# Kernel tuning notes

Hardware: AMD Instinct MI355X
Metric: run time of the kernel (lower is better)

Reference implementation:

```python
import jax, jax.numpy as jnp
import numpy as np
jax.config.update('jax_enable_x64', True)

B, S, D, H, V, P = 4, 2048, 512, 8, 100000, 256
NGRAMS = list(range(3, 9))  # n-gram lengths 3..8
DH = D // H
SCALE = np.float32(DH ** -0.5)

def _layernorm(x, g, b, eps=1e-5):
    m = jnp.mean(x, -1, keepdims=True)
    v = jnp.mean(jnp.square(x - m), -1, keepdims=True)
    return g * (x - m) / jnp.sqrt(v + eps) + b

def _mha(q, k, v, Wq, bq, Wk, bk, Wv, bv, Wo, bo):
    Bq, Lq, _ = q.shape
    qh = (q @ Wq + bq).reshape(Bq, Lq, H, DH)
    kh = (k @ Wk + bk).reshape(Bq, -1, H, DH)
    vh = (v @ Wv + bv).reshape(Bq, -1, H, DH)
    s = jnp.einsum('bqhd,bkhd->bhqk', qh, kh) * SCALE
    a = jax.nn.softmax(s, axis=-1)
    o = jnp.einsum('bhqk,bkhd->bqhd', a, vh).reshape(Bq, Lq, D)
    return o @ Wo + bo

def _ngram_hash(bytes_seq, n):
    # hash[:, i] = sum_k bytes[:, i-n+1+k] * 256**k for i >= n-1 else 0, then mod V
    # (int64 wraparound for n=8 matches torch semantics)
    b = bytes_seq.astype(jnp.int64)
    h = jnp.zeros_like(b)
    for k in range(n):
        shift = n - 1 - k
        shifted = jnp.pad(b, ((0, 0), (shift, 0)))[:, :S]
        h = h + shifted * (256 ** k)
    h = jnp.where(jnp.arange(S) >= (n - 1), h, 0)
    return h % V

def _forward(bytes_seq, patch_idx, byte_emb, ngram_emb, sWq, sbq, sWk, sbk, sWv, sbv, sWo, sbo, ln1g, ln1b, W1, b1, W2, b2, ln2g, ln2b, cWq, cbq, cWk, cbk, cWv, cbv, cWo, cbo):
    embeds = byte_emb[bytes_seq]  # [B,S,D]
    for j, n in enumerate(NGRAMS):
        embeds = embeds + ngram_emb[j][_ngram_hash(bytes_seq, n)]
    embeds = embeds / np.float32(len(NGRAMS) + 1)
    # one post-norm transformer encoder layer (relu FFN, eval mode / no dropout)
    x = _layernorm(embeds + _mha(embeds, embeds, embeds, sWq, sbq, sWk, sbk, sWv, sbv, sWo, sbo), ln1g, ln1b)
    ff = jax.nn.relu(x @ W1 + b1) @ W2 + b2
    x = _layernorm(x + ff, ln2g, ln2b)
    # gather patch-boundary queries per batch, cross-attend to full sequence
    q = jnp.take_along_axis(x, patch_idx[..., None], axis=1)  # [B,P,D]
    return _mha(q, x, x, cWq, cbq, cWk, cbk, cWv, cbv, cWo, cbo)

def setup_inputs():
    key = jax.random.key(0)
    ks = jax.random.split(key, 20)
    f32 = jnp.float32
    def rn(k, shape, scale=0.02):
        return (jax.random.normal(k, shape, f32) * scale).astype(f32)
    return {
        'bytes_seq': jax.random.randint(ks[0], (B, S), 0, 256, dtype=jnp.int64),
        'patch_idx': jnp.sort(jax.random.randint(ks[1], (B, P), 0, S, dtype=jnp.int64), axis=1),
        'byte_emb': rn(ks[2], (256, D)),
        'ngram_emb': rn(ks[3], (len(NGRAMS), V, D)),
        'sWq': rn(ks[4], (D, D)), 'sbq': jnp.zeros((D,), f32),
        'sWk': rn(ks[5], (D, D)), 'sbk': jnp.zeros((D,), f32),
        'sWv': rn(ks[6], (D, D)), 'sbv': jnp.zeros((D,), f32),
        'sWo': rn(ks[7], (D, D)), 'sbo': jnp.zeros((D,), f32),
        'ln1g': jnp.ones((D,), f32), 'ln1b': jnp.zeros((D,), f32),
        'W1': rn(ks[8], (D, 4 * D)), 'b1': jnp.zeros((4 * D,), f32),
        'W2': rn(ks[9], (4 * D, D)), 'b2': jnp.zeros((D,), f32),
        'ln2g': jnp.ones((D,), f32), 'ln2b': jnp.zeros((D,), f32),
        'cWq': rn(ks[10], (D, D)), 'cbq': jnp.zeros((D,), f32),
        'cWk': rn(ks[11], (D, D)), 'cbk': jnp.zeros((D,), f32),
        'cWv': rn(ks[12], (D, D)), 'cbv': jnp.zeros((D,), f32),
        'cWo': rn(ks[13], (D, D)), 'cbo': jnp.zeros((D,), f32),
    }

def reference(bytes_seq, patch_idx, byte_emb, ngram_emb, sWq, sbq, sWk, sbk, sWv, sbv, sWo, sbo, ln1g, ln1b, W1, b1, W2, b2, ln2g, ln2b, cWq, cbq, cWk, cbk, cWv, cbv, cWo, cbo):
    return _forward(bytes_seq, patch_idx, byte_emb, ngram_emb, sWq, sbq, sWk, sbk, sWv, sbv, sWo, sbo, ln1g, ln1b, W1, b1, W2, b2, ln2g, ln2b, cWq, cbq, cWk, cbk, cWv, cbv, cWo, cbo)
```

## Files before the change

kernel.cpp:

```cpp
#include <hip/hip_runtime.h>
#include <stdint.h>

#define B_   4
#define S_   2048
#define D_   512
#define H_   8
#define DH_  64
#define V_   100000
#define P_   256
#define N_   (B_*S_)
#define NP_  (B_*P_)

typedef _Float16 f16;
typedef _Float16 f16x8 __attribute__((ext_vector_type(8)));
typedef float    f32x4 __attribute__((ext_vector_type(4)));
typedef uint32_t u32x4 __attribute__((ext_vector_type(4)));

#define MFMA16(a,b,c) __builtin_amdgcn_mfma_f32_16x16x32_f16((a),(b),(c),0,0,0)
#define GLDS16(gp, lp) __builtin_amdgcn_global_load_lds( \
    (const __attribute__((address_space(1))) void*)(gp), \
    (__attribute__((address_space(3))) void*)(lp), 16, 0, 0)

__global__ __launch_bounds__(128) void embed_kernel(
    const int* __restrict__ bytes_seq, const float* __restrict__ byte_emb,
    const float* __restrict__ ngram_emb, f16* __restrict__ out16)
{
  const int pos = blockIdx.x;
  const int b = pos / S_, s = pos % S_;
  const int* bs = bytes_seq + (size_t)b * S_;

  int w[8];
  #pragma unroll
  for (int k = 0; k < 8; k++) {
    int p = s - 7 + k;
    w[k] = (p >= 0) ? bs[p] : 0;
  }

  int idx[6];
  #pragma unroll
  for (int j = 0; j < 6; j++) {
    const int n = j + 3;
    int id = 0;
    if (s >= n - 1) {
      uint64_t h = 0;
      for (int k = 0; k < n; k++)
        h += (uint64_t)(uint32_t)w[8 - n + k] << (8 * k);
      long long sh = (long long)h;
      long long r = sh % (long long)V_;
      if (r < 0) r += V_;
      id = (int)r;
    }
    idx[j] = id;
  }

  const int d = threadIdx.x * 4;
  float4 acc = *(const float4*)(byte_emb + (size_t)bs[s] * D_ + d);
  #pragma unroll
  for (int j = 0; j < 6; j++) {
    const float4 v = *(const float4*)(ngram_emb + ((size_t)j * V_ + idx[j]) * D_ + d);
    acc.x += v.x; acc.y += v.y; acc.z += v.z; acc.w += v.w;
  }
  const float inv7 = 1.0f / 7.0f;
  f16* o16 = out16 + (size_t)pos * D_ + d;
  f16 t4[4];
  t4[0] = (f16)(acc.x * inv7); t4[1] = (f16)(acc.y * inv7);
  t4[2] = (f16)(acc.z * inv7); t4[3] = (f16)(acc.w * inv7);
  *(uint2*)o16 = *(uint2*)t4;
}

struct WJobs {
  const float* src[10];
  f16* dst[10];
  int K[10], N[10], tiles[10];
};

__global__ __launch_bounds__(256) void wconv_kernel(WJobs jobs,
    const float* sbq, const float* sbk, const float* sbv,
    const float* cbk, const float* cbv, float* bqkv, float* bckv)
{
  const int j = blockIdx.y;
  const int tile = blockIdx.x;
  if (j == 0 && tile >= jobs.tiles[0] && tile < jobs.tiles[0] + 10) {
    int t = (tile - jobs.tiles[0]) * 256 + threadIdx.x;
    if (t < 512)       bqkv[t] = sbq[t];
    else if (t < 1024) bqkv[t] = sbk[t - 512];
    else if (t < 1536) bqkv[t] = sbv[t - 1024];
    else if (t < 2048) bckv[t - 1536] = cbk[t - 1536];
    else if (t < 2560) bckv[t - 1536] = cbv[t - 2048];
    return;
  }
  if (tile >= jobs.tiles[j]) return;
  const int K = jobs.K[j], N = jobs.N[j];
  const int ntiles = N >> 5;
  const int kt = (tile / ntiles) << 5, nt = (tile % ntiles) << 5;
  __shared__ float T[32][33];
  const int t = threadIdx.x;
  const float* src = jobs.src[j];
  #pragma unroll
  for (int p = 0; p < 4; p++) {
    int lin = t + p * 256;
    int rr = lin >> 5, cc = lin & 31;
    T[rr][cc] = src[(size_t)(kt + rr) * N + nt + cc];
  }
  __syncthreads();
  f16* dst = jobs.dst[j];
  #pragma unroll
  for (int p = 0; p < 4; p++) {
    int lin = t + p * 256;
    int rr = lin >> 5, cc = lin & 31;
    dst[(size_t)(nt + rr) * K + kt + cc] = (f16)T[cc][rr];
  }
}

template<typename OutT, int RELU, int BN>
__global__ __launch_bounds__(256) void gemm_f16(
    const f16* __restrict__ A, const f16* __restrict__ Bt,
    const float* __restrict__ bias, OutT* __restrict__ C,
    int M, int N, int K, const int* __restrict__ rowmap)
{
  constexpr int NF = BN / 32;
  __shared__ __align__(16) f16 As[2][128 * 32];
  __shared__ __align__(16) f16 Bs[2][BN * 32];
  const int tid = threadIdx.x;
  const int l = tid & 63;
  const int lo4 = l & 15, hi2 = l >> 4;
  const int w = tid >> 6;
  const int wr = w >> 1, wc = w & 1;
  const int bm = blockIdx.x * 128, bn = blockIdx.y * BN;

  size_t aoff[2];
  #pragma unroll
  for (int i = 0; i < 2; i++) {
    int r = bm + i * 64 + (tid >> 2);
    int ar = rowmap ? ((r >> 8) * S_ + rowmap[r]) : r;
    aoff[i] = (size_t)ar * K + (tid & 3) * 8;
  }

  f32x4 acc[4][NF];
  #pragma unroll
  for (int m = 0; m < 4; m++)
    #pragma unroll
    for (int n = 0; n < NF; n++) acc[m][n] = (f32x4){0.f, 0.f, 0.f, 0.f};

  const int nt = K >> 5;

  #pragma unroll
  for (int i = 0; i < 2; i++)
    GLDS16(A + aoff[i], &As[0][(i * 256 + tid) * 8]);
  #pragma unroll
  for (int i = 0; i < BN / 64; i++) {
    int c = i * 256 + tid;
    GLDS16(Bt + (size_t)(bn + (c >> 2)) * K + (c & 3) * 8, &Bs[0][c * 8]);
  }

  for (int t = 0; t < nt; t++) {
    __syncthreads();
    const int cur = t & 1;
    if (t + 1 < nt) {
      const int k0 = (t + 1) << 5;
      #pragma unroll
      for (int i = 0; i < 2; i++)
        GLDS16(A + aoff[i] + k0, &As[cur ^ 1][(i * 256 + tid) * 8]);
      #pragma unroll
      for (int i = 0; i < BN / 64; i++) {
        int c = i * 256 + tid;
        GLDS16(Bt + (size_t)(bn + (c >> 2)) * K + k0 + (c & 3) * 8, &Bs[cur ^ 1][c * 8]);
      }
    }
    f16x8 af[4], bf[NF];
    const f16* pa = &As[cur][(wr * 64 + lo4) * 32 + hi2 * 8];
    const f16* pb = &Bs[cur][(wc * (BN / 2) + lo4) * 32 + hi2 * 8];
    #pragma unroll
    for (int m = 0; m < 4; m++) af[m] = *(const f16x8*)(pa + m * 16 * 32);
    #pragma unroll
    for (int n = 0; n < NF; n++) bf[n] = *(const f16x8*)(pb + n * 16 * 32);
    #pragma unroll
    for (int m = 0; m < 4; m++)
      #pragma unroll
      for (int n = 0; n < NF; n++)
        acc[m][n] = MFMA16(af[m], bf[n], acc[m][n]);
  }

  #pragma unroll
  for (int n = 0; n < NF; n++) {
    const int col = bn + wc * (BN / 2) + n * 16 + lo4;
    const float bcol = bias[col];
    #pragma unroll
    for (int m = 0; m < 4; m++) {
      const int row0 = bm + wr * 64 + m * 16 + hi2 * 4;
      #pragma unroll
      for (int j = 0; j < 4; j++) {
        float v = acc[m][n][j] + bcol;
        if (RELU) v = fmaxf(v, 0.f);
        C[(size_t)(row0 + j) * N + col] = (OutT)v;
      }
    }
  }
}

template<int QG>
__global__ __launch_bounds__(256) void attn_f16(
    const f16* __restrict__ Q, int qs,
    const f16* __restrict__ Kp, const f16* __restrict__ Vp, int kvs,
    f16* __restrict__ O, int NQ)
{
  __shared__ __align__(16) f16 Ks[2][64][76];
  __shared__ __align__(16) f16 Vt[2][64][76];

  const int tid = threadIdx.x;
  const int w = tid >> 6, l = tid & 63;
  const int lo4 = l & 15, hi2 = l >> 4;
  const int lin = blockIdx.x;
  const int h = lin & 7, b = (lin >> 3) & 3, qt = lin >> 5;

  const f16 qscale = (f16)0.18033688f;
  f16x8 qf[QG][2];
  #pragma unroll
  for (int qg = 0; qg < QG; qg++) {
    const int qrow = qt * (64 * QG) + w * (16 * QG) + qg * 16 + lo4;
    const f16* Qp = Q + (size_t)(b * NQ + qrow) * qs + h * DH_ + hi2 * 8;
    qf[qg][0] = *(const f16x8*)(Qp);
    qf[qg][1] = *(const f16x8*)(Qp + 32);
    #pragma unroll
    for (int i = 0; i < 8; i++) { qf[qg][0][i] *= qscale; qf[qg][1][i] *= qscale; }
  }

  const int g2 = lo4 >> 2, j4 = lo4 & 3;
  const int kvp0 = 8 * g2 + j4;
  const int kvp1 = 8 * (g2 ^ 2) + 4 + j4;
  const int pidx = (l ^ 32) << 2;

  const f16* Kb = Kp + (size_t)b * S_ * kvs + h * DH_;
  const f16* Vb = Vp + (size_t)b * S_ * kvs + h * DH_;

  float lsum[QG];
  f32x4 oacc[QG][4];
  #pragma unroll
  for (int qg = 0; qg < QG; qg++) {
    lsum[qg] = 0.f;
    #pragma unroll
    for (int df = 0; df < 4; df++) oacc[qg][df] = (f32x4){0.f, 0.f, 0.f, 0.f};
  }

  const int r0 = tid >> 3;
  const int c8 = tid & 7;

  f16x8 kreg[2], vreg[2];
  #pragma unroll
  for (int i = 0; i < 2; i++) {
    int row = i * 32 + r0;
    kreg[i] = *(const f16x8*)(Kb + (size_t)row * kvs + c8 * 8);
    vreg[i] = *(const f16x8*)(Vb + (size_t)row * kvs + c8 * 8);
  }
  #pragma unroll
  for (int i = 0; i < 2; i++) {
    int row = i * 32 + r0;
    *(f16x8*)(&Ks[0][row][c8 * 8]) = kreg[i];
    #pragma unroll
    for (int jj = 0; jj < 8; jj++) Vt[0][c8 * 8 + jj][row] = vreg[i][jj];
  }
  __syncthreads();

  const int NT = S_ / 64;
  int cur = 0;
  for (int t = 0; t < NT; t++) {
    if (t + 1 < NT) {
      #pragma unroll
      for (int i = 0; i < 2; i++) {
        int row = (t + 1) * 64 + i * 32 + r0;
        kreg[i] = *(const f16x8*)(Kb + (size_t)row * kvs + c8 * 8);
        vreg[i] = *(const f16x8*)(Vb + (size_t)row * kvs + c8 * 8);
      }
    }
    f32x4 sacc[QG][4];
    #pragma unroll
    for (int nf = 0; nf < 4; nf++) {
      const int krow = ((nf & 1) ? kvp1 : kvp0) + (nf >> 1) * 32;
      f16x8 kf0 = *(const f16x8*)(&Ks[cur][krow][hi2 * 8]);
      f16x8 kf1 = *(const f16x8*)(&Ks[cur][krow][32 + hi2 * 8]);
      #pragma unroll
      for (int qg = 0; qg < QG; qg++) {
        f32x4 s = (f32x4){0.f, 0.f, 0.f, 0.f};
        s = MFMA16(kf0, qf[qg][0], s);
        s = MFMA16(kf1, qf[qg][1], s);
        sacc[qg][nf] = s;
      }
    }
    uint32_t packs[QG][4][2];
    #pragma unroll
    for (int qg = 0; qg < QG; qg++)
      #pragma unroll
      for (int nf = 0; nf < 4; nf++) {
        float p0 = exp2f(fminf(sacc[qg][nf][0], 15.f));
        float p1 = exp2f(fminf(sacc[qg][nf][1], 15.f));
        float p2 = exp2f(fminf(sacc[qg][nf][2], 15.f));
        float p3 = exp2f(fminf(sacc[qg][nf][3], 15.f));
        lsum[qg] += (p0 + p1) + (p2 + p3);
        packs[qg][nf][0] = __builtin_bit_cast(uint32_t, __builtin_amdgcn_cvt_pkrtz(p0, p1));
        packs[qg][nf][1] = __builtin_bit_cast(uint32_t, __builtin_amdgcn_cvt_pkrtz(p2, p3));
      }
    #pragma unroll
    for (int ks = 0; ks < 2; ks++) {
      f16x8 pb[QG];
      #pragma unroll
      for (int qg = 0; qg < QG; qg++) {
        uint32_t w0 = packs[qg][2 * ks][0];
        uint32_t w1 = packs[qg][2 * ks][1];
        uint32_t w2 = (uint32_t)__builtin_amdgcn_ds_bpermute(pidx, (int)packs[qg][2 * ks + 1][0]);
        uint32_t w3 = (uint32_t)__builtin_amdgcn_ds_bpermute(pidx, (int)packs[qg][2 * ks + 1][1]);
        u32x4 bw = (u32x4){w0, w1, w2, w3};
        pb[qg] = __builtin_bit_cast(f16x8, bw);
      }
      #pragma unroll
      for (int df = 0; df < 4; df++) {
        f16x8 vf = *(const f16x8*)(&Vt[cur][df * 16 + lo4][ks * 32 + hi2 * 8]);
        #pragma unroll
        for (int qg = 0; qg < QG; qg++)
          oacc[qg][df] = MFMA16(vf, pb[qg], oacc[qg][df]);
      }
    }
    if (t + 1 < NT) {
      #pragma unroll
      for (int i = 0; i < 2; i++) {
        int row = i * 32 + r0;
        *(f16x8*)(&Ks[cur ^ 1][row][c8 * 8]) = kreg[i];
        #pragma unroll
        for (int jj = 0; jj < 8; jj++) Vt[cur ^ 1][c8 * 8 + jj][row] = vreg[i][jj];
      }
    }
    __syncthreads();
    cur ^= 1;
  }

  #pragma unroll
  for (int qg = 0; qg < QG; qg++) {
    float r = lsum[qg];
    r += __shfl_xor(r, 16, 64);
    r += __shfl_xor(r, 32, 64);
    const float invl = 1.0f / r;
    const int orow = qt * (64 * QG) + w * (16 * QG) + qg * 16 + lo4;
    f16* Ob = O + (size_t)(b * NQ + orow) * D_ + h * DH_ + hi2 * 4;
    #pragma unroll
    for (int df = 0; df < 4; df++) {
      f16 t4[4];
      #pragma unroll
      for (int j = 0; j < 4; j++) t4[j] = (f16)(oacc[qg][df][j] * invl);
      *(uint2*)(Ob + df * 16) = *(uint2*)t4;
    }
  }
}

__global__ __launch_bounds__(128) void ln_kernel(
    const f16* __restrict__ a, const f16* __restrict__ r,
    const float* __restrict__ g, const float* __restrict__ be,
    f16* __restrict__ out)
{
  const int row = blockIdx.x;
  const int t = threadIdx.x;
  const f16* ap = a + (size_t)row * D_ + t * 4;
  const f16* rp = r + (size_t)row * D_ + t * 4;
  uint2 au = *(const uint2*)ap, ru = *(const uint2*)rp;
  f16 a4[4], r4[4];
  *(uint2*)a4 = au; *(uint2*)r4 = ru;
  float x0 = (float)a4[0] + (float)r4[0];
  float x1 = (float)a4[1] + (float)r4[1];
  float x2 = (float)a4[2] + (float)r4[2];
  float x3 = (float)a4[3] + (float)r4[3];
  float sm = x0 + x1 + x2 + x3;
  float sq = x0*x0 + x1*x1 + x2*x2 + x3*x3;
  #pragma unroll
  for (int off = 32; off > 0; off >>= 1) {
    sm += __shfl_down(sm, off, 64);
    sq += __shfl_down(sq, off, 64);
  }
  __shared__ float s0[2], s1[2];
  if ((t & 63) == 0) { s0[t >> 6] = sm; s1[t >> 6] = sq; }
  __syncthreads();
  const float Sm = s0[0] + s0[1];
  const float Sq = s1[0] + s1[1];
  const float mean = Sm * (1.0f / 512.0f);
  const float var  = Sq * (1.0f / 512.0f) - mean * mean;
  const float inv  = rsqrtf(var + 1e-5f);
  const float4 vg = *(const float4*)(g + t * 4);
  const float4 vb = *(const float4*)(be + t * 4);
  f16 o4[4];
  o4[0] = (f16)(vg.x * (x0 - mean) * inv + vb.x);
  o4[1] = (f16)(vg.y * (x1 - mean) * inv + vb.y);
  o4[2] = (f16)(vg.z * (x2 - mean) * inv + vb.z);
  o4[3] = (f16)(vg.w * (x3 - mean) * inv + vb.w);
  *(uint2*)(out + (size_t)row * D_ + t * 4) = *(uint2*)o4;
}

extern "C" void kernel_launch(void* const* d_in, const int* in_sizes, int n_in,
                              void* d_out, int out_size, void* d_ws, size_t ws_size,
                              hipStream_t stream) {
  const int*   bytes_seq = (const int*)  d_in[0];
  const int*   patch_idx = (const int*)  d_in[1];
  const float* byte_emb  = (const float*)d_in[2];
  const float* ngram_emb = (const float*)d_in[3];
  const float* sWq = (const float*)d_in[4];  const float* sbq = (const float*)d_in[5];
  const float* sWk = (const float*)d_in[6];  const float* sbk = (const float*)d_in[7];
  const float* sWv = (const float*)d_in[8];  const float* sbv = (const float*)d_in[9];
  const float* sWo = (const float*)d_in[10]; const float* sbo = (const float*)d_in[11];
  const float* ln1g = (const float*)d_in[12]; const float* ln1b = (const float*)d_in[13];
  const float* W1 = (const float*)d_in[14];  const float* b1 = (const float*)d_in[15];
  const float* W2 = (const float*)d_in[16];  const float* b2 = (const float*)d_in[17];
  const float* ln2g = (const float*)d_in[18]; const float* ln2b = (const float*)d_in[19];
  const float* cWq = (const float*)d_in[20]; const float* cbq = (const float*)d_in[21];
  const float* cWk = (const float*)d_in[22]; const float* cbk = (const float*)d_in[23];
  const float* cWv = (const float*)d_in[24]; const float* cbv = (const float*)d_in[25];
  const float* cWo = (const float*)d_in[26]; const float* cbo = (const float*)d_in[27];

  char* base = (char*)d_ws;
  const size_t MB = 1u << 20;
  f16* E16     = (f16*)(base + 0 * MB);
  f16* TMP16   = (f16*)(base + 8 * MB);
  f16* X116    = (f16*)(base + 16 * MB);
  f16* X216    = (f16*)(base + 24 * MB);
  f16* QKV16   = (f16*)(base + 32 * MB);
  f16* AT16    = (f16*)(base + 56 * MB);
  f16* HID16   = (f16*)(base + 64 * MB);
  f16* CKV16   = (f16*)(base + 96 * MB);
  f16* CQ16    = (f16*)(base + 112 * MB);
  f16* CO16    = (f16*)(base + 113 * MB);
  f16* WT      = (f16*)(base + 114 * MB);
  float* bqkv  = (float*)(base + 123 * MB);
  float* bckv  = bqkv + 1536;

  f16* QKVT = WT;
  f16* sWoT = QKVT + 786432;
  f16* W1T  = sWoT + 262144;
  f16* W2T  = W1T + 1048576;
  f16* cWqT = W2T + 1048576;
  f16* CKVT = cWqT + 262144;
  f16* cWoT = CKVT + 524288;

  WJobs wj;
  {
    const float* wsrc[10] = {sWq, sWk, sWv, sWo, W1, W2, cWq, cWk, cWv, cWo};
    f16* wdst[10] = {QKVT, QKVT + 262144, QKVT + 524288, sWoT, W1T, W2T,
                     cWqT, CKVT, CKVT + 262144, cWoT};
    const int wK[10] = {512,512,512,512, 512,2048, 512,512,512,512};
    const int wN[10] = {512,512,512,512, 2048,512, 512,512,512,512};
    for (int i = 0; i < 10; i++) {
      wj.src[i] = wsrc[i]; wj.dst[i] = wdst[i];
      wj.K[i] = wK[i]; wj.N[i] = wN[i];
      wj.tiles[i] = (wK[i] >> 5) * (wN[i] >> 5);
    }
  }

  const dim3 blk256(256), blk128(128);

  wconv_kernel<<<dim3(1024, 10), blk256, 0, stream>>>(wj, sbq, sbk, sbv, cbk, cbv, bqkv, bckv);
  embed_kernel<<<N_, blk128, 0, stream>>>(bytes_seq, byte_emb, ngram_emb, E16);

  gemm_f16<f16, 0, 128><<<dim3(64, 12), blk256, 0, stream>>>(E16, QKVT, bqkv, QKV16, N_, 1536, 512, nullptr);

  attn_f16<2><<<512, blk256, 0, stream>>>(QKV16, 1536, QKV16 + 512, QKV16 + 1024, 1536, AT16, S_);

  gemm_f16<f16, 0, 64><<<dim3(64, 8), blk256, 0, stream>>>(AT16, sWoT, sbo, TMP16, N_, 512, 512, nullptr);
  ln_kernel<<<N_, blk128, 0, stream>>>(E16, TMP16, ln1g, ln1b, X116);

  gemm_f16<f16, 1, 128><<<dim3(64, 16), blk256, 0, stream>>>(X116, W1T, b1, HID16, N_, 2048, 512, nullptr);
  gemm_f16<f16, 0, 64><<<dim3(64, 8), blk256, 0, stream>>>(HID16, W2T, b2, TMP16, N_, 512, 2048, nullptr);
  ln_kernel<<<N_, blk128, 0, stream>>>(X116, TMP16, ln2g, ln2b, X216);

  gemm_f16<f16, 0, 128><<<dim3(64, 8), blk256, 0, stream>>>(X216, CKVT, bckv, CKV16, N_, 1024, 512, nullptr);
  gemm_f16<f16, 0, 64><<<dim3(8, 8), blk256, 0, stream>>>(X216, cWqT, cbq, CQ16, NP_, 512, 512, patch_idx);
  attn_f16<1><<<128, blk256, 0, stream>>>(CQ16, 512, CKV16, CKV16 + 512, 1024, CO16, P_);

  gemm_f16<float, 0, 64><<<dim3(8, 8), blk256, 0, stream>>>(CO16, cWoT, cbo, (float*)d_out, NP_, 512, 512, nullptr);
}
```

Baseline: 287.4 us.

## Emit transposed V from GEMM epilogue, merge prep and cross-attn projection kernels

The QKV and cross-KV GEMM epilogues now write V in a per-(batch,head) transposed layout, so the attention kernel loads V tiles straight into LDS with global_load_lds and an XOR swizzle. This replaces the register round trip and scalar transposed LDS stores it used before. Weight conversion, bias copy and embedding are merged into one prep kernel, and the cross K/V and Q projections share one launch. The cost is extra workspace and scattered 8-byte stores in the GEMM epilogue.

```diff
diff --git a/kernel.cpp b/kernel.cpp
--- a/kernel.cpp
+++ b/kernel.cpp
@@ -21,11 +21,58 @@
     (const __attribute__((address_space(1))) void*)(gp), \
     (__attribute__((address_space(3))) void*)(lp), 16, 0, 0)
 
-__global__ __launch_bounds__(128) void embed_kernel(
+struct WJobs {
+  const float* src[10];
+  f16* dst[10];
+  int K[10], N[10], tiles[10];
+};
+
+__global__ __launch_bounds__(256) void prep_kernel(WJobs jobs,
+    const float* __restrict__ sbq, const float* __restrict__ sbk,
+    const float* __restrict__ sbv, const float* __restrict__ cbk,
+    const float* __restrict__ cbv, float* __restrict__ bqkv,
+    float* __restrict__ bckv,
     const int* __restrict__ bytes_seq, const float* __restrict__ byte_emb,
     const float* __restrict__ ngram_emb, f16* __restrict__ out16)
 {
-  const int pos = blockIdx.x;
+  int bid = blockIdx.x;
+  if (bid < 10240) {
+    const int j = bid >> 10, tile = bid & 1023;
+    if (tile >= jobs.tiles[j]) return;
+    const int K = jobs.K[j], N = jobs.N[j];
+    const int ntiles = N >> 5;
+    const int kt = (tile / ntiles) << 5, nt = (tile % ntiles) << 5;
+    __shared__ float T[32][33];
+    const int t = threadIdx.x;
+    const float* src = jobs.src[j];
+    #pragma unroll
+    for (int p = 0; p < 4; p++) {
+      int lin = t + p * 256;
+      int rr = lin >> 5, cc = lin & 31;
+      T[rr][cc] = src[(size_t)(kt + rr) * N + nt + cc];
+    }
+    __syncthreads();
+    f16* dst = jobs.dst[j];
+    #pragma unroll
+    for (int p = 0; p < 4; p++) {
+      int lin = t + p * 256;
+      int rr = lin >> 5, cc = lin & 31;
+      dst[(size_t)(nt + rr) * K + kt + cc] = (f16)T[cc][rr];
+    }
+    return;
+  }
+  bid -= 10240;
+  if (bid < 10) {
+    int t = bid * 256 + threadIdx.x;
+    if (t < 512)       bqkv[t] = sbq[t];
+    else if (t < 1024) bqkv[t] = sbk[t - 512];
+    else if (t < 1536) bqkv[t] = sbv[t - 1024];
+    else if (t < 2048) bckv[t - 1536] = cbk[t - 1536];
+    else if (t < 2560) bckv[t - 1536] = cbv[t - 2048];
+    return;
+  }
+  bid -= 10;
+  const int pos = bid * 2 + (threadIdx.x >> 7);
   const int b = pos / S_, s = pos % S_;
   const int* bs = bytes_seq + (size_t)b * S_;
 
@@ -35,7 +82,6 @@
     int p = s - 7 + k;
     w[k] = (p >= 0) ? bs[p] : 0;
   }
-
   int idx[6];
   #pragma unroll
   for (int j = 0; j < 6; j++) {
@@ -52,8 +98,7 @@
     }
     idx[j] = id;
   }
-
-  const int d = threadIdx.x * 4;
+  const int d = (threadIdx.x & 127) * 4;
   float4 acc = *(const float4*)(byte_emb + (size_t)bs[s] * D_ + d);
   #pragma unroll
   for (int j = 0; j < 6; j++) {
@@ -61,62 +106,18 @@
     acc.x += v.x; acc.y += v.y; acc.z += v.z; acc.w += v.w;
   }
   const float inv7 = 1.0f / 7.0f;
-  f16* o16 = out16 + (size_t)pos * D_ + d;
   f16 t4[4];
   t4[0] = (f16)(acc.x * inv7); t4[1] = (f16)(acc.y * inv7);
   t4[2] = (f16)(acc.z * inv7); t4[3] = (f16)(acc.w * inv7);
-  *(uint2*)o16 = *(uint2*)t4;
-}
-
-struct WJobs {
-  const float* src[10];
-  f16* dst[10];
-  int K[10], N[10], tiles[10];
-};
-
-__global__ __launch_bounds__(256) void wconv_kernel(WJobs jobs,
-    const float* sbq, const float* sbk, const float* sbv,
-    const float* cbk, const float* cbv, float* bqkv, float* bckv)
-{
-  const int j = blockIdx.y;
-  const int tile = blockIdx.x;
-  if (j == 0 && tile >= jobs.tiles[0] && tile < jobs.tiles[0] + 10) {
-    int t = (tile - jobs.tiles[0]) * 256 + threadIdx.x;
-    if (t < 512)       bqkv[t] = sbq[t];
-    else if (t < 1024) bqkv[t] = sbk[t - 512];
-    else if (t < 1536) bqkv[t] = sbv[t - 1024];
-    else if (t < 2048) bckv[t - 1536] = cbk[t - 1536];
-    else if (t < 2560) bckv[t - 1536] = cbv[t - 2048];
-    return;
-  }
-  if (tile >= jobs.tiles[j]) return;
-  const int K = jobs.K[j], N = jobs.N[j];
-  const int ntiles = N >> 5;
-  const int kt = (tile / ntiles) << 5, nt = (tile % ntiles) << 5;
-  __shared__ float T[32][33];
-  const int t = threadIdx.x;
-  const float* src = jobs.src[j];
-  #pragma unroll
-  for (int p = 0; p < 4; p++) {
-    int lin = t + p * 256;
-    int rr = lin >> 5, cc = lin & 31;
-    T[rr][cc] = src[(size_t)(kt + rr) * N + nt + cc];
-  }
-  __syncthreads();
-  f16* dst = jobs.dst[j];
-  #pragma unroll
-  for (int p = 0; p < 4; p++) {
-    int lin = t + p * 256;
-    int rr = lin >> 5, cc = lin & 31;
-    dst[(size_t)(nt + rr) * K + kt + cc] = (f16)T[cc][rr];
-  }
-}
-
-template<typename OutT, int RELU, int BN>
-__global__ __launch_bounds__(256) void gemm_f16(
+  *(uint2*)(out16 + (size_t)pos * D_ + d) = *(uint2*)t4;
+}
+
+template<typename OutT, int RELU, int BN, int VTSTART>
+__device__ __forceinline__ void gemm_body(
     const f16* __restrict__ A, const f16* __restrict__ Bt,
     const float* __restrict__ bias, OutT* __restrict__ C,
-    int M, int N, int K, const int* __restrict__ rowmap)
+    int M, int N, int K, const int* __restrict__ rowmap,
+    f16* __restrict__ vt, int bmi, int bni)
 {
   constexpr int NF = BN / 32;
   __shared__ __align__(16) f16 As[2][128 * 32];
@@ -126,7 +127,7 @@
   const int lo4 = l & 15, hi2 = l >> 4;
   const int w = tid >> 6;
   const int wr = w >> 1, wc = w & 1;
-  const int bm = blockIdx.x * 128, bn = blockIdx.y * BN;
+  const int bm = bmi * 128, bn = bni * BN;
 
   size_t aoff[2];
   #pragma unroll
@@ -181,6 +182,27 @@
         acc[m][n] = MFMA16(af[m], bf[n], acc[m][n]);
   }
 
+  if constexpr (VTSTART >= 0) {
+    if (bn >= VTSTART) {
+      #pragma unroll
+      for (int n = 0; n < NF; n++) {
+        const int col = bn + wc * (BN / 2) + n * 16 + lo4;
+        const float bcol = bias[col];
+        const int dcol = col - VTSTART;
+        const size_t vbase = ((size_t)(dcol >> 6) * 64 + (dcol & 63)) << 11;
+        #pragma unroll
+        for (int m = 0; m < 4; m++) {
+          const int row0 = bm + wr * 64 + m * 16 + hi2 * 4;
+          f16 t4[4];
+          #pragma unroll
+          for (int j = 0; j < 4; j++) t4[j] = (f16)(acc[m][n][j] + bcol);
+          *(uint2*)(vt + (((size_t)(row0 >> 11) * 8) << 17) + vbase + (row0 & 2047)) = *(uint2*)t4;
+        }
+      }
+      return;
+    }
+  }
+
   #pragma unroll
   for (int n = 0; n < NF; n++) {
     const int col = bn + wc * (BN / 2) + n * 16 + lo4;
@@ -198,14 +220,42 @@
   }
 }
 
+template<typename OutT, int RELU, int BN, int VTSTART>
+__global__ __launch_bounds__(256) void gemm_f16(
+    const f16* __restrict__ A, const f16* __restrict__ Bt,
+    const float* __restrict__ bias, OutT* __restrict__ C,
+    int M, int N, int K, const int* __restrict__ rowmap, f16* __restrict__ vt)
+{
+  gemm_body<OutT, RELU, BN, VTSTART>(A, Bt, bias, C, M, N, K, rowmap, vt,
+                                     blockIdx.x, blockIdx.y);
+}
+
+__global__ __launch_bounds__(256) void ckv_cq_kernel(
+    const f16* __restrict__ X, const f16* __restrict__ CKVT,
+    const float* __restrict__ bckv, f16* __restrict__ CKV,
+    f16* __restrict__ vt2, const f16* __restrict__ cWqT,
+    const float* __restrict__ cbq, f16* __restrict__ CQ,
+    const int* __restrict__ pidx)
+{
+  int bid = blockIdx.x;
+  if (bid < 512) {
+    gemm_body<f16, 0, 128, 512>(X, CKVT, bckv, CKV, N_, 1024, 512,
+                                nullptr, vt2, bid >> 3, bid & 7);
+  } else {
+    bid -= 512;
+    gemm_body<f16, 0, 64, -1>(X, cWqT, cbq, CQ, NP_, 512, 512,
+                              pidx, nullptr, bid >> 3, bid & 7);
+  }
+}
+
 template<int QG>
 __global__ __launch_bounds__(256) void attn_f16(
     const f16* __restrict__ Q, int qs,
-    const f16* __restrict__ Kp, const f16* __restrict__ Vp, int kvs,
-    f16* __restrict__ O, int NQ)
+    const f16* __restrict__ Kp, int kvs,
+    const f16* __restrict__ VT, f16* __restrict__ O, int NQ)
 {
   __shared__ __align__(16) f16 Ks[2][64][76];
-  __shared__ __align__(16) f16 Vt[2][64][76];
+  __shared__ __align__(16) f16 VtL[2][64 * 64];
 
   const int tid = threadIdx.x;
   const int w = tid >> 6, l = tid & 63;
@@ -229,9 +279,10 @@
   const int kvp0 = 8 * g2 + j4;
   const int kvp1 = 8 * (g2 ^ 2) + 4 + j4;
   const int pidx = (l ^ 32) << 2;
+  const int vswz = lo4 & 7;
 
   const f16* Kb = Kp + (size_t)b * S_ * kvs + h * DH_;
-  const f16* Vb = Vp + (size_t)b * S_ * kvs + h * DH_;
+  const f16* VTbh = VT + (((size_t)(b * 8 + h)) << 17);
 
   float lsum[QG];
   f32x4 oacc[QG][4];
@@ -244,33 +295,37 @@
 
   const int r0 = tid >> 3;
   const int c8 = tid & 7;
-
-  f16x8 kreg[2], vreg[2];
+  const int vr = tid >> 3;
+  const int vch = tid & 7;
+
   #pragma unroll
   for (int i = 0; i < 2; i++) {
-    int row = i * 32 + r0;
-    kreg[i] = *(const f16x8*)(Kb + (size_t)row * kvs + c8 * 8);
-    vreg[i] = *(const f16x8*)(Vb + (size_t)row * kvs + c8 * 8);
-  }
-  #pragma unroll
-  for (int i = 0; i < 2; i++) {
-    int row = i * 32 + r0;
-    *(f16x8*)(&Ks[0][row][c8 * 8]) = kreg[i];
-    #pragma unroll
-    for (int jj = 0; jj < 8; jj++) Vt[0][c8 * 8 + jj][row] = vreg[i][jj];
-  }
+    int r = i * 32 + vr, ch = vch;
+    GLDS16(VTbh + (size_t)r * 2048 + ((ch ^ (r & 7)) * 8), &VtL[0][(i * 256 + tid) * 8]);
+  }
+  f16x8 kreg[2];
+  #pragma unroll
+  for (int i = 0; i < 2; i++)
+    kreg[i] = *(const f16x8*)(Kb + (size_t)(i * 32 + r0) * kvs + c8 * 8);
+  #pragma unroll
+  for (int i = 0; i < 2; i++)
+    *(f16x8*)(&Ks[0][i * 32 + r0][c8 * 8]) = kreg[i];
   __syncthreads();
 
   const int NT = S_ / 64;
   int cur = 0;
   for (int t = 0; t < NT; t++) {
     if (t + 1 < NT) {
+      const int kt2 = (t + 1) * 64;
       #pragma unroll
       for (int i = 0; i < 2; i++) {
-        int row = (t + 1) * 64 + i * 32 + r0;
-        kreg[i] = *(const f16x8*)(Kb + (size_t)row * kvs + c8 * 8);
-        vreg[i] = *(const f16x8*)(Vb + (size_t)row * kvs + c8 * 8);
-      }
+        int r = i * 32 + vr;
+        GLDS16(VTbh + (size_t)r * 2048 + kt2 + ((vch ^ (r & 7)) * 8),
+               &VtL[cur ^ 1][(i * 256 + tid) * 8]);
+      }
+      #pragma unroll
+      for (int i = 0; i < 2; i++)
+        kreg[i] = *(const f16x8*)(Kb + (size_t)(kt2 + i * 32 + r0) * kvs + c8 * 8);
     }
     f32x4 sacc[QG][4];
     #pragma unroll
@@ -313,7 +368,9 @@
       }
       #pragma unroll
       for (int df = 0; df < 4; df++) {
-        f16x8 vf = *(const f16x8*)(&Vt[cur][df * 16 + lo4][ks * 32 + hi2 * 8]);
+        const int r = df * 16 + lo4;
+        const int cc = (ks * 4 + hi2) ^ vswz;
+        f16x8 vf = *(const f16x8*)(&VtL[cur][r * 64 + cc * 8]);
         #pragma unroll
         for (int qg = 0; qg < QG; qg++)
           oacc[qg][df] = MFMA16(vf, pb[qg], oacc[qg][df]);
@@ -321,12 +378,8 @@
     }
     if (t + 1 < NT) {
       #pragma unroll
-      for (int i = 0; i < 2; i++) {
-        int row = i * 32 + r0;
-        *(f16x8*)(&Ks[cur ^ 1][row][c8 * 8]) = kreg[i];
-        #pragma unroll
-        for (int jj = 0; jj < 8; jj++) Vt[cur ^ 1][c8 * 8 + jj][row] = vreg[i][jj];
-      }
+      for (int i = 0; i < 2; i++)
+        *(f16x8*)(&Ks[cur ^ 1][i * 32 + r0][c8 * 8]) = kreg[i];
     }
     __syncthreads();
     cur ^= 1;
@@ -426,6 +479,8 @@
   f16* WT      = (f16*)(base + 114 * MB);
   float* bqkv  = (float*)(base + 123 * MB);
   float* bckv  = bqkv + 1536;
+  f16* VT      = (f16*)(base + 124 * MB);
+  f16* VT2     = (f16*)(base + 132 * MB);
 
   f16* QKVT = WT;
   f16* sWoT = QKVT + 786432;
@@ -451,23 +506,29 @@
 
   const dim3 blk256(256), blk128(128);
 
-  wconv_kernel<<<dim3(1024, 10), blk256, 0, stream>>>(wj, sbq, sbk, sbv, cbk, cbv, bqkv, bckv);
-  embed_kernel<<<N_, blk128, 0, stream>>>(bytes_seq, byte_emb, ngram_emb, E16);
-
-  gemm_f16<f16, 0, 128><<<dim3(64, 12), blk256, 0, stream>>>(E16, QKVT, bqkv, QKV16, N_, 1536, 512, nullptr);
-
-  attn_f16<2><<<512, blk256, 0, stream>>>(QKV16, 1536, QKV16 + 512, QKV16 + 1024, 1536, AT16, S_);
-
-  gemm_f16<f16, 0, 64><<<dim3(64, 8), blk256, 0, stream>>>(AT16, sWoT, sbo, TMP16, N_, 512, 512, nullptr);
+  prep_kernel<<<10240 + 10 + 4096, blk256, 0, stream>>>(
+      wj, sbq, sbk, sbv, cbk, cbv, bqkv, bckv,
+      bytes_seq, byte_emb, ngram_emb, E16);
+
+  gemm_f16<f16, 0, 128, 1024><<<dim3(64, 12), blk256, 0, stream>>>(
+      E16, QKVT, bqkv, QKV16, N_, 1536, 512, nullptr, VT);
+
+  attn_f16<2><<<512, blk256, 0, stream>>>(QKV16, 1536, QKV16 + 512, 1536, VT, AT16, S_);
+
+  gemm_f16<f16, 0, 64, -1><<<dim3(64, 8), blk256, 0, stream>>>(
+      AT16, sWoT, sbo, TMP16, N_, 512, 512, nullptr, nullptr);
   ln_kernel<<<N_, blk128, 0, stream>>>(E16, TMP16, ln1g, ln1b, X116);
 
-  gemm_f16<f16, 1, 128><<<dim3(64, 16), blk256, 0, stream>>>(X116, W1T, b1, HID16, N_, 2048, 512, nullptr);
-  gemm_f16<f16, 0, 64><<<dim3(64, 8), blk256, 0, stream>>>(HID16, W2T, b2, TMP16, N_, 512, 2048, nullptr);
+  gemm_f16<f16, 1, 128, -1><<<dim3(64, 16), blk256, 0, stream>>>(
+      X116, W1T, b1, HID16, N_, 2048, 512, nullptr, nullptr);
+  gemm_f16<f16, 0, 64, -1><<<dim3(64, 8), blk256, 0, stream>>>(
+      HID16, W2T, b2, TMP16, N_, 512, 2048, nullptr, nullptr);
   ln_kernel<<<N_, blk128, 0, stream>>>(X116, TMP16, ln2g, ln2b, X216);
 
-  gemm_f16<f16, 0, 128><<<dim3(64, 8), blk256, 0, stream>>>(X216, CKVT, bckv, CKV16, N_, 1024, 512, nullptr);
-  gemm_f16<f16, 0, 64><<<dim3(8, 8), blk256, 0, stream>>>(X216, cWqT, cbq, CQ16, NP_, 512, 512, patch_idx);
-  attn_f16<1><<<128, blk256, 0, stream>>>(CQ16, 512, CKV16, CKV16 + 512, 1024, CO16, P_);
-
-  gemm_f16<float, 0, 64><<<dim3(8, 8), blk256, 0, stream>>>(CO16, cWoT, cbo, (float*)d_out, NP_, 512, 512, nullptr);
-}
+  ckv_cq_kernel<<<576, blk256, 0, stream>>>(
+      X216, CKVT, bckv, CKV16, VT2, cWqT, cbq, CQ16, patch_idx);
+  attn_f16<1><<<128, blk256, 0, stream>>>(CQ16, 512, CKV16, 1024, VT2, CO16, P_);
+
+  gemm_f16<float, 0, 64, -1><<<dim3(8, 8), blk256, 0, stream>>>(
+      CO16, cWoT, cbo, (float*)d_out, NP_, 512, 512, nullptr, nullptr);
+}
```

New measurement: 289.6 us. Within noise of the previous version (+0.7%).
